# Performance work log

Measured on AMD Instinct MI355X. Metric: run time of the kernel, lower is better.

The kernel has to match this reference:

```python
import jax, jax.numpy as jnp
import numpy as np
import math

B, S, HID = 2, 2048, 2048
NH, NKV = 32, 8
HD = HID // NH  # 64
N_REP = NH // NKV  # 4


def setup_inputs() -> dict:
    key = jax.random.key(0)
    ks = jax.random.split(key, 7)
    sc = 0.02
    return {
        "hidden_states": jax.random.normal(ks[0], (B, S, HID), jnp.float32),
        "cos": jax.random.normal(ks[1], (S, HD), jnp.float32),
        "sin": jax.random.normal(ks[2], (S, HD), jnp.float32),
        "wq": jax.random.normal(ks[3], (NH * HD, HID), jnp.float32) * sc,
        "wk": jax.random.normal(ks[4], (NKV * HD, HID), jnp.float32) * sc,
        "wv": jax.random.normal(ks[5], (NKV * HD, HID), jnp.float32) * sc,
        "wo": jax.random.normal(ks[6], (HID, NH * HD), jnp.float32) * sc,
    }


def _rotate_half(x):
    x1, x2 = jnp.split(x, 2, axis=-1)
    return jnp.concatenate([-x2, x1], axis=-1)


def _apply_rotary(q, k, cos, sin):
    # q: [B,S,NH,HD], k: [B,S,NKV,HD]; cos/sin: [S,HD] broadcast over batch, heads
    c = cos[None, :, None, :]
    s = sin[None, :, None, :]
    return q * c + _rotate_half(q) * s, k * c + _rotate_half(k) * s


def reference(hidden_states, cos, sin, wq, wk, wv, wo):
    x = hidden_states  # [B,S,HID]
    q = jnp.einsum('bsh,dh->bsd', x, wq).reshape(B, S, NH, HD)
    k = jnp.einsum('bsh,dh->bsd', x, wk).reshape(B, S, NKV, HD)
    v = jnp.einsum('bsh,dh->bsd', x, wv).reshape(B, S, NKV, HD)
    q, k = _apply_rotary(q, k, cos, sin)
    # repeat_kv: expand kv heads by N_REP -> [B,S,NH,HD]
    k = jnp.repeat(k, N_REP, axis=2)
    v = jnp.repeat(v, N_REP, axis=2)
    # [B,NH,S,HD]
    q = q.transpose(0, 2, 1, 3)
    k = k.transpose(0, 2, 1, 3)
    v = v.transpose(0, 2, 1, 3)
    scores = jnp.einsum('bhqd,bhkd->bhqk', q, k) / math.sqrt(HD)
    probs = jax.nn.softmax(scores.astype(jnp.float32), axis=-1).astype(q.dtype)
    out = jnp.einsum('bhqk,bhkd->bhqd', probs, v)
    out = out.transpose(0, 2, 1, 3).reshape(B, S, NH * HD)
    return jnp.einsum('bsd,hd->bsh', out, wo)
```

## Files before the change

kernel.cpp:

```cpp
#include <hip/hip_runtime.h>
#include <math.h>

#define B 2
#define S 2048
#define HID 2048
#define NH 32
#define NKV 8
#define HD 64
#define NREP 4

typedef __bf16 bf16_t;
typedef bf16_t bf16x8 __attribute__((ext_vector_type(8)));
typedef bf16_t bf16x4 __attribute__((ext_vector_type(4)));
typedef bf16_t bf16x2 __attribute__((ext_vector_type(2)));
typedef float floatx4 __attribute__((ext_vector_type(4)));

__device__ __forceinline__ void gld_lds16(const void* g, void* l) {
    __builtin_amdgcn_global_load_lds(
        (const __attribute__((address_space(1))) void*)g,
        (__attribute__((address_space(3))) void*)l, 16, 0, 0);
}

__device__ __forceinline__ int pack2(float a, float b) {
    bf16x2 v; v[0] = (bf16_t)a; v[1] = (bf16_t)b;
    return __builtin_bit_cast(int, v);
}

__device__ __forceinline__ bf16x8 cat8i(int2 lo, int2 hi) {
    int4 w; w.x = lo.x; w.y = lo.y; w.z = hi.x; w.w = hi.y;
    return __builtin_bit_cast(bf16x8, w);
}

__global__ __launch_bounds__(256) void cast_all(const float* __restrict__ x,
                                                const float* __restrict__ wq,
                                                const float* __restrict__ wk,
                                                const float* __restrict__ wv,
                                                const float* __restrict__ wo,
                                                bf16_t* __restrict__ xb,
                                                bf16_t* __restrict__ wqkvb,
                                                bf16_t* __restrict__ wob) {
    int gid = blockIdx.x * 256 + threadIdx.x;
    const float* src; bf16_t* dst; int idx;
    if (gid < 1048576)      { src = x;  dst = xb;               idx = gid; }
    else if (gid < 1572864) { src = wq; dst = wqkvb;            idx = gid - 1048576; }
    else if (gid < 1703936) { src = wk; dst = wqkvb + 4194304;  idx = gid - 1572864; }
    else if (gid < 1835008) { src = wv; dst = wqkvb + 5242880;  idx = gid - 1703936; }
    else                    { src = wo; dst = wob;              idx = gid - 1835008; }
    size_t i = (size_t)idx * 8;
    float4 f0 = *(const float4*)(src + i);
    float4 f1 = *(const float4*)(src + i + 4);
    bf16x8 v;
    v[0] = (bf16_t)f0.x; v[1] = (bf16_t)f0.y; v[2] = (bf16_t)f0.z; v[3] = (bf16_t)f0.w;
    v[4] = (bf16_t)f1.x; v[5] = (bf16_t)f1.y; v[6] = (bf16_t)f1.z; v[7] = (bf16_t)f1.w;
    *(bf16x8*)(dst + i) = v;
}

#define TM 128
#define TN 128
#define BK 64

enum { MODE_QKV = 0, MODE_OUT = 2 };

template <int MODE>
__global__ __launch_bounds__(256) void gemm_mfma(const bf16_t* __restrict__ A,
                                                 const bf16_t* __restrict__ W,
                                                 void* __restrict__ outQ,
                                                 bf16_t* __restrict__ outK,
                                                 bf16_t* __restrict__ outV,
                                                 const float* __restrict__ cosp,
                                                 const float* __restrict__ sinp,
                                                 int M, int N, int K) {
    __shared__ __align__(16) bf16_t As[2 * TM * 32];
    __shared__ __align__(16) bf16_t Ws[2 * TN * 32];
    const int t    = threadIdx.x;
    const int wave = t >> 6, lane = t & 63;
    const int quad = lane >> 4, l16 = lane & 15;
    const int m0 = blockIdx.y * TM, n0 = blockIdx.x * TN;
    const int wm = (wave >> 1) * 64, wn = (wave & 1) * 64;

    floatx4 zero4 = {0.f, 0.f, 0.f, 0.f};
    floatx4 acc[4][4];
    #pragma unroll
    for (int i = 0; i < 4; ++i)
        #pragma unroll
        for (int j = 0; j < 4; ++j) acc[i][j] = zero4;

    const int r4 = t >> 2;
    const int c8 = (t & 3) * 8;
    const bf16_t* Arow = A + (size_t)(m0 + r4) * K + c8;
    const bf16_t* Wrow = W + (size_t)(n0 + r4) * K + c8;

    for (int k0 = 0; k0 < K; k0 += BK) {
        #pragma unroll
        for (int ks = 0; ks < 2; ++ks) {
            gld_lds16(Arow + k0 + ks * 32,          As + ks * 4096 + t * 8);
            gld_lds16(Arow + 64 * K + k0 + ks * 32, As + ks * 4096 + 2048 + t * 8);
            gld_lds16(Wrow + k0 + ks * 32,          Ws + ks * 4096 + t * 8);
            gld_lds16(Wrow + 64 * K + k0 + ks * 32, Ws + ks * 4096 + 2048 + t * 8);
        }
        __syncthreads();
        #pragma unroll
        for (int ks = 0; ks < 2; ++ks) {
            bf16x8 af[4], bfr[4];
            #pragma unroll
            for (int i = 0; i < 4; ++i)
                af[i] = *(bf16x8*)&As[ks * 4096 + (wm + i * 16 + l16) * 32 + quad * 8];
            #pragma unroll
            for (int j = 0; j < 4; ++j)
                bfr[j] = *(bf16x8*)&Ws[ks * 4096 + (wn + j * 16 + l16) * 32 + quad * 8];
            #pragma unroll
            for (int i = 0; i < 4; ++i)
                #pragma unroll
                for (int j = 0; j < 4; ++j)
                    acc[i][j] = __builtin_amdgcn_mfma_f32_16x16x32_bf16(af[i], bfr[j], acc[i][j], 0, 0, 0);
        }
        __syncthreads();
    }

    if constexpr (MODE == MODE_OUT) {
        float* C = (float*)outQ;
        #pragma unroll
        for (int i = 0; i < 4; ++i)
            #pragma unroll
            for (int r = 0; r < 4; ++r) {
                int row = m0 + wm + i * 16 + quad * 4 + r;
                #pragma unroll
                for (int j = 0; j < 4; ++j)
                    C[(size_t)row * N + n0 + wn + j * 16 + l16] = acc[i][j][r];
            }
    } else {
        const int hh = (n0 + wn) / 64;
        #pragma unroll
        for (int i = 0; i < 4; ++i)
            #pragma unroll
            for (int r = 0; r < 4; ++r) {
                int m = m0 + wm + i * 16 + quad * 4 + r;
                int b = m / S, s = m % S;
                if (hh < NH + NKV) {
                    bf16_t* base;
                    float sc;
                    if (hh < NH) {
                        base = (bf16_t*)outQ + ((size_t)(b * NH + hh) * S + s) * HD;
                        sc = 0.18033688011f;
                    } else {
                        base = outK + ((size_t)(b * NKV + (hh - NH)) * S + s) * HD;
                        sc = 1.0f;
                    }
                    #pragma unroll
                    for (int j = 0; j < 2; ++j) {
                        int d = j * 16 + l16;
                        float x1 = acc[i][j][r], x2 = acc[i][j + 2][r];
                        float c1 = cosp[s * HD + d],      s1 = sinp[s * HD + d];
                        float c2 = cosp[s * HD + d + 32], s2 = sinp[s * HD + d + 32];
                        base[d]      = (bf16_t)((x1 * c1 - x2 * s1) * sc);
                        base[d + 32] = (bf16_t)((x2 * c2 + x1 * s2) * sc);
                    }
                } else {
                    int kvh = hh - NH - NKV;
                    int w  = s & 63, lo = w & 31;
                    int pos = (lo < 16) ? (((lo >> 2) << 3) | (lo & 3))
                                        : ((((lo - 16) >> 2) << 3) | 4 | (lo & 3));
                    int ps = (s & ~63) | ((w & 32) + pos);
                    bf16_t* vb = outV + ((size_t)(b * NKV + kvh) * HD) * S + ps;
                    #pragma unroll
                    for (int j = 0; j < 4; ++j)
                        vb[(size_t)(j * 16 + l16) * S] = (bf16_t)acc[i][j][r];
                }
            }
    }
}

__global__ __launch_bounds__(512, 2) void attn_mfma(const bf16_t* __restrict__ Q,
                                                    const bf16_t* __restrict__ Kb,
                                                    const bf16_t* __restrict__ Vt,
                                                    bf16_t* __restrict__ Ob) {
    __shared__ __align__(16) bf16_t Ks[2][64][32];
    __shared__ __align__(16) bf16_t Vs[2][64][32];
    const int t    = threadIdx.x;
    const int wave = t >> 6, lane = t & 63;
    const int quad = lane >> 4, l16 = lane & 15;

    const int flat  = blockIdx.y * 16 + blockIdx.x;
    const int local = flat >> 3;
    const int combo = (flat & 7) * 2 + (local >> 4);
    const int b = combo >> 3, kvh = combo & 7;
    const int q0 = (local & 15) * 128;
    const int h  = kvh * NREP + (wave & 3);
    const int qw = q0 + (wave >> 2) * 64;

    const bf16_t* qbase = Q + ((size_t)(b * NH + h) * S + qw) * HD;
    const bf16_t* kbase = Kb + ((size_t)(b * NKV + kvh) * S) * HD;
    const bf16_t* vbase = Vt + (size_t)(b * NKV + kvh) * HD * S;

    bf16x8 qf[4][2];
    #pragma unroll
    for (int qj = 0; qj < 4; ++qj)
        #pragma unroll
        for (int ks = 0; ks < 2; ++ks)
            qf[qj][ks] = *(const bf16x8*)(qbase + (size_t)(qj * 16 + l16) * HD + ks * 32 + quad * 8);

    floatx4 zero4 = {0.f, 0.f, 0.f, 0.f};
    floatx4 of[4][4];
    #pragma unroll
    for (int di = 0; di < 4; ++di)
        #pragma unroll
        for (int qj = 0; qj < 4; ++qj) of[di][qj] = zero4;
    float lsum[4] = {0.f, 0.f, 0.f, 0.f};

    const int sp = t >> 8;
    const int sr = (t >> 2) & 63;
    const int sc = (t & 3) * 8;

    gld_lds16(kbase + (size_t)sr * HD + sp * 32 + sc, (bf16_t*)Ks + t * 8);
    __syncthreads();

    for (int kt = 0; kt < S; kt += 64) {
        gld_lds16(vbase + (size_t)sr * S + kt + sp * 32 + sc, (bf16_t*)Vs + t * 8);

        int2 pk[4][4];
        #pragma unroll
        for (int ki = 0; ki < 4; ++ki) {
            bf16x8 ka0 = *(bf16x8*)&Ks[0][ki * 16 + l16][quad * 8];
            bf16x8 ka1 = *(bf16x8*)&Ks[1][ki * 16 + l16][quad * 8];
            floatx4 sf[4];
            #pragma unroll
            for (int qj = 0; qj < 4; ++qj) sf[qj] = zero4;
            __builtin_amdgcn_s_setprio(1);
            #pragma unroll
            for (int qj = 0; qj < 4; ++qj)
                sf[qj] = __builtin_amdgcn_mfma_f32_16x16x32_bf16(ka0, qf[qj][0], sf[qj], 0, 0, 0);
            #pragma unroll
            for (int qj = 0; qj < 4; ++qj)
                sf[qj] = __builtin_amdgcn_mfma_f32_16x16x32_bf16(ka1, qf[qj][1], sf[qj], 0, 0, 0);
            __builtin_amdgcn_s_setprio(0);
            #pragma unroll
            for (int qj = 0; qj < 4; ++qj) {
                float p0 = __builtin_amdgcn_exp2f(sf[qj][0]);
                float p1 = __builtin_amdgcn_exp2f(sf[qj][1]);
                float p2 = __builtin_amdgcn_exp2f(sf[qj][2]);
                float p3 = __builtin_amdgcn_exp2f(sf[qj][3]);
                lsum[qj] += (p0 + p1) + (p2 + p3);
                pk[ki][qj].x = pack2(p0, p1);
                pk[ki][qj].y = pack2(p2, p3);
            }
        }
        __syncthreads();

        if (kt + 64 < S)
            gld_lds16(kbase + (size_t)(kt + 64 + sr) * HD + sp * 32 + sc, (bf16_t*)Ks + t * 8);
        #pragma unroll
        for (int ks = 0; ks < 2; ++ks) {
            __builtin_amdgcn_s_setprio(1);
            #pragma unroll
            for (int di = 0; di < 4; ++di) {
                bf16x8 va = *(bf16x8*)&Vs[ks][di * 16 + l16][quad * 8];
                #pragma unroll
                for (int qj = 0; qj < 4; ++qj) {
                    bf16x8 pb = cat8i(pk[2 * ks][qj], pk[2 * ks + 1][qj]);
                    of[di][qj] = __builtin_amdgcn_mfma_f32_16x16x32_bf16(va, pb, of[di][qj], 0, 0, 0);
                }
            }
            __builtin_amdgcn_s_setprio(0);
        }
        __syncthreads();
    }

    #pragma unroll
    for (int qj = 0; qj < 4; ++qj) {
        float ls = lsum[qj];
        ls += __shfl_xor(ls, 16);
        ls += __shfl_xor(ls, 32);
        float inv = 1.f / ls;
        int q = qw + qj * 16 + l16;
        bf16_t* ob = Ob + ((size_t)(b * S + q)) * HID + h * HD;
        #pragma unroll
        for (int di = 0; di < 4; ++di) {
            int2 pkv;
            pkv.x = pack2(of[di][qj][0] * inv, of[di][qj][1] * inv);
            pkv.y = pack2(of[di][qj][2] * inv, of[di][qj][3] * inv);
            *(int2*)(ob + di * 16 + quad * 4) = pkv;
        }
    }
}

extern "C" void kernel_launch(void* const* d_in, const int* in_sizes, int n_in,
                              void* d_out, int out_size, void* d_ws, size_t ws_size,
                              hipStream_t stream) {
    const float* x    = (const float*)d_in[0];
    const float* cosp = (const float*)d_in[1];
    const float* sinp = (const float*)d_in[2];
    const float* wq   = (const float*)d_in[3];
    const float* wk   = (const float*)d_in[4];
    const float* wv   = (const float*)d_in[5];
    const float* wo   = (const float*)d_in[6];
    float* out = (float*)d_out;

    char* ws = (char*)d_ws;
    bf16_t* xb    = (bf16_t*)(ws);
    bf16_t* kb    = (bf16_t*)(ws + 16777216);
    bf16_t* vtb   = (bf16_t*)(ws + 20971520);
    bf16_t* wqkvb = (bf16_t*)(ws + 25165824);
    bf16_t* wob   = (bf16_t*)(ws + 37748736);
    bf16_t* attb  = (bf16_t*)(ws);
    bf16_t* qb    = (bf16_t*)d_out;

    const int M = B * S;

    cast_all<<<9216, 256, 0, stream>>>(x, wq, wk, wv, wo, xb, wqkvb, wob);

    gemm_mfma<MODE_QKV><<<dim3(3072 / TN, M / TM), 256, 0, stream>>>(
        xb, wqkvb, (void*)qb, kb, vtb, cosp, sinp, M, 3072, HID);

    attn_mfma<<<dim3(16, 16), 512, 0, stream>>>(qb, kb, vtb, attb);

    gemm_mfma<MODE_OUT><<<dim3(2048 / TN, M / TM), 256, 0, stream>>>(
        attb, wob, (void*)out, nullptr, nullptr, nullptr, nullptr, M, 2048, HID);
}
```

Baseline: 310.1 us.

## Double-buffer K/V tiles in attention and shrink blocks to 256 threads

The attention kernel now keeps two LDS buffers for both K and V and prefetches the next 64-key tile while computing the current one, dropping one of the two barriers per iteration. Blocks shrink from 512 to 256 threads (4 waves, one per head in the GQA group, 64 queries), and the grid doubles to keep coverage. This targets the exposed global-load latency and barrier stalls, at the cost of reusing each K/V tile across half as many query rows, so K/V traffic doubles.

```diff
diff --git a/kernel.cpp b/kernel.cpp
--- a/kernel.cpp
+++ b/kernel.cpp
@@ -170,25 +170,24 @@
     }
 }
 
-__global__ __launch_bounds__(512, 2) void attn_mfma(const bf16_t* __restrict__ Q,
+__global__ __launch_bounds__(256, 2) void attn_mfma(const bf16_t* __restrict__ Q,
                                                     const bf16_t* __restrict__ Kb,
                                                     const bf16_t* __restrict__ Vt,
                                                     bf16_t* __restrict__ Ob) {
-    __shared__ __align__(16) bf16_t Ks[2][64][32];
-    __shared__ __align__(16) bf16_t Vs[2][64][32];
+    __shared__ __align__(16) bf16_t Ks[2][2][64][32];
+    __shared__ __align__(16) bf16_t Vs[2][2][64][32];
     const int t    = threadIdx.x;
     const int wave = t >> 6, lane = t & 63;
     const int quad = lane >> 4, l16 = lane & 15;
 
     const int flat  = blockIdx.y * 16 + blockIdx.x;
     const int local = flat >> 3;
-    const int combo = (flat & 7) * 2 + (local >> 4);
+    const int combo = (flat & 7) * 2 + (local >> 5);
     const int b = combo >> 3, kvh = combo & 7;
-    const int q0 = (local & 15) * 128;
-    const int h  = kvh * NREP + (wave & 3);
-    const int qw = q0 + (wave >> 2) * 64;
-
-    const bf16_t* qbase = Q + ((size_t)(b * NH + h) * S + qw) * HD;
+    const int q0 = (local & 31) * 64;
+    const int h  = kvh * NREP + wave;
+
+    const bf16_t* qbase = Q + ((size_t)(b * NH + h) * S + q0) * HD;
     const bf16_t* kbase = Kb + ((size_t)(b * NKV + kvh) * S) * HD;
     const bf16_t* vbase = Vt + (size_t)(b * NKV + kvh) * HD * S;
 
@@ -207,21 +206,33 @@
         for (int qj = 0; qj < 4; ++qj) of[di][qj] = zero4;
     float lsum[4] = {0.f, 0.f, 0.f, 0.f};
 
-    const int sp = t >> 8;
-    const int sr = (t >> 2) & 63;
-    const int sc = (t & 3) * 8;
-
-    gld_lds16(kbase + (size_t)sr * HD + sp * 32 + sc, (bf16_t*)Ks + t * 8);
+    const int r4 = t >> 2;
+    const int c8 = (t & 3) * 8;
+
+    #pragma unroll
+    for (int ks = 0; ks < 2; ++ks) {
+        gld_lds16(kbase + (size_t)r4 * HD + ks * 32 + c8, &Ks[0][ks][0][0] + t * 8);
+        gld_lds16(vbase + (size_t)r4 * S + ks * 32 + c8,  &Vs[0][ks][0][0] + t * 8);
+    }
     __syncthreads();
 
+    int cur = 0;
     for (int kt = 0; kt < S; kt += 64) {
-        gld_lds16(vbase + (size_t)sr * S + kt + sp * 32 + sc, (bf16_t*)Vs + t * 8);
+        if (kt + 64 < S) {
+            #pragma unroll
+            for (int ks = 0; ks < 2; ++ks) {
+                gld_lds16(kbase + (size_t)(kt + 64 + r4) * HD + ks * 32 + c8,
+                          &Ks[cur ^ 1][ks][0][0] + t * 8);
+                gld_lds16(vbase + (size_t)r4 * S + kt + 64 + ks * 32 + c8,
+                          &Vs[cur ^ 1][ks][0][0] + t * 8);
+            }
+        }
 
         int2 pk[4][4];
         #pragma unroll
         for (int ki = 0; ki < 4; ++ki) {
-            bf16x8 ka0 = *(bf16x8*)&Ks[0][ki * 16 + l16][quad * 8];
-            bf16x8 ka1 = *(bf16x8*)&Ks[1][ki * 16 + l16][quad * 8];
+            bf16x8 ka0 = *(bf16x8*)&Ks[cur][0][ki * 16 + l16][quad * 8];
+            bf16x8 ka1 = *(bf16x8*)&Ks[cur][1][ki * 16 + l16][quad * 8];
             floatx4 sf[4];
             #pragma unroll
             for (int qj = 0; qj < 4; ++qj) sf[qj] = zero4;
@@ -244,16 +255,13 @@
                 pk[ki][qj].y = pack2(p2, p3);
             }
         }
-        __syncthreads();
-
-        if (kt + 64 < S)
-            gld_lds16(kbase + (size_t)(kt + 64 + sr) * HD + sp * 32 + sc, (bf16_t*)Ks + t * 8);
+
         #pragma unroll
         for (int ks = 0; ks < 2; ++ks) {
             __builtin_amdgcn_s_setprio(1);
             #pragma unroll
             for (int di = 0; di < 4; ++di) {
-                bf16x8 va = *(bf16x8*)&Vs[ks][di * 16 + l16][quad * 8];
+                bf16x8 va = *(bf16x8*)&Vs[cur][ks][di * 16 + l16][quad * 8];
                 #pragma unroll
                 for (int qj = 0; qj < 4; ++qj) {
                     bf16x8 pb = cat8i(pk[2 * ks][qj], pk[2 * ks + 1][qj]);
@@ -262,7 +270,9 @@
             }
             __builtin_amdgcn_s_setprio(0);
         }
+
         __syncthreads();
+        cur ^= 1;
     }
 
     #pragma unroll
@@ -271,7 +281,7 @@
         ls += __shfl_xor(ls, 16);
         ls += __shfl_xor(ls, 32);
         float inv = 1.f / ls;
-        int q = qw + qj * 16 + l16;
+        int q = q0 + qj * 16 + l16;
         bf16_t* ob = Ob + ((size_t)(b * S + q)) * HID + h * HD;
         #pragma unroll
         for (int di = 0; di < 4; ++di) {
@@ -311,7 +321,7 @@
     gemm_mfma<MODE_QKV><<<dim3(3072 / TN, M / TM), 256, 0, stream>>>(
         xb, wqkvb, (void*)qb, kb, vtb, cosp, sinp, M, 3072, HID);
 
-    attn_mfma<<<dim3(16, 16), 512, 0, stream>>>(qb, kb, vtb, attb);
+    attn_mfma<<<dim3(16, 32), 256, 0, stream>>>(qb, kb, vtb, attb);
 
     gemm_mfma<MODE_OUT><<<dim3(2048 / TN, M / TM), 256, 0, stream>>>(
         attb, wob, (void*)out, nullptr, nullptr, nullptr, nullptr, M, 2048, HID);
```

New measurement: 315.7 us. About the same (+1.8%).
